# Optimization experiments

Hardware: AMD Instinct MI355X
Metric: run time of the kernel (lower is better)

## Reference

```python
import jax, jax.numpy as jnp
import numpy as np

B, MD, N = 8, 256, 4096          # batch, model_dim, n_points
H, F, S = 8, 16, 32              # heads, in_feature_dim, tensor_size (3D lattice S^3)
EPS = 1e-5


def _bn(x, g, b):
    # training-mode BatchNorm1d over (batch, points), x: [B, C, N]
    m = x.mean(axis=(0, 2), keepdims=True)
    v = x.var(axis=(0, 2), keepdims=True)
    return (x - m) * jax.lax.rsqrt(v + EPS) * g[None, :, None] + b[None, :, None]


def setup_inputs() -> dict:
    key = jax.random.key(0)
    ks = jax.random.split(key, 10)
    return {
        "x": jax.random.normal(ks[0], (B, MD, N), jnp.float32),
        "pcd": jax.random.uniform(ks[1], (B, 3, N), jnp.float32, -1.0, 1.0),
        "W_kv": jax.random.normal(ks[2], (H * (F + 3), MD), jnp.float32) / np.float32(np.sqrt(MD)),
        "key_gamma": 0.1 * jax.random.normal(ks[3], (H * 3,), jnp.float32),
        "key_beta": jnp.zeros((H * 3,), jnp.float32),
        "val_gamma": jnp.ones((H * F,), jnp.float32) + 0.1 * jax.random.normal(ks[4], (H * F,), jnp.float32),
        "val_beta": jnp.zeros((H * F,), jnp.float32),
        "R": jnp.tile(jnp.eye(3, dtype=jnp.float32), (H, 1, 1)) + 0.05 * jax.random.normal(ks[5], (H, 3, 3), jnp.float32),
        "t": 0.05 * jax.random.normal(ks[6], (H, 3), jnp.float32),
        "conv_w": jax.random.normal(ks[7], (H * F, F, 3, 3, 3), jnp.float32) / np.float32(np.sqrt(F * 27)),
        "conv_b": jnp.zeros((H * F,), jnp.float32),
        "after_gamma": jnp.ones((H * F,), jnp.float32),
        "after_beta": jnp.zeros((H * F,), jnp.float32),
    }


# precomputed 8 trilinear corner offsets
_OFFS = np.array([[dx, dy, dz] for dx in (0, 1) for dy in (0, 1) for dz in (0, 1)])
_OFF_FLAT = jnp.asarray((_OFFS[:, 0] * S + _OFFS[:, 1]) * S + _OFFS[:, 2], jnp.int32)  # [8]
_OFF_BOOL = jnp.asarray(_OFFS.astype(bool))  # [8, 3]


def _forward(x, pcd, W_kv, key_gamma, key_beta, val_gamma, val_beta, R, t,
             conv_w, conv_b, after_gamma, after_beta):
    # keys/values prediction (1x1 conv == matmul)
    kv = jnp.einsum('om,bmn->bon', W_kv, x)                      # [B, H*(F+3), N]
    keys_res = _bn(kv[:, :H * 3], key_gamma, key_beta).reshape(B, H, 3, N)
    values = _bn(kv[:, H * 3:], val_gamma, val_beta)              # [B, H*F, N]
    # per-head learned affine transform of shifted point coords (VolTransformer)
    keys = jnp.einsum('hij,bhjn->bhin', R, pcd[:, None] + keys_res) + t[None, :, :, None]
    lattice = jnp.tanh(keys)                                      # [B, H, 3, N] in (-1, 1)
    # DifferentiablePositions: map to lattice coords, split into floor index + frac
    pos = (lattice + 1.0) * 0.5 * (S - 1)
    fl_f = jnp.clip(jnp.floor(pos), 0.0, S - 2.0)
    frac = pos - fl_f                                             # differentiable local coords
    fl = fl_f.astype(jnp.int32)
    base = (fl[:, :, 0] * S + fl[:, :, 1]) * S + fl[:, :, 2]      # [B, H, N] flattened index
    idx8 = base[:, :, None, :] + _OFF_FLAT[None, None, :, None]   # [B, H, 8, N]
    # trilinear corner weights: prod_d (frac_d if corner bit else 1-frac_d)
    w8 = jnp.prod(jnp.where(_OFF_BOOL[None, None, :, :, None],
                            frac[:, :, None], 1.0 - frac[:, :, None]), axis=3)  # [B, H, 8, N]
    # Splat: weighted scatter-add onto the lattice
    vals = values.reshape(B, H, F, N)
    contrib = (vals[:, :, :, None, :] * w8[:, :, None]).reshape(B * H, F, 8 * N)
    idx_f = idx8.reshape(B * H, 8 * N)
    z = jax.vmap(lambda c, i: jnp.zeros((F, S ** 3), c.dtype).at[:, i].add(c))(contrib, idx_f)
    z = z.reshape(B, H * F, S, S, S)
    # heads-grouped 3x3x3 conv over the lattice
    zc = jax.lax.conv_general_dilated(
        z, conv_w, window_strides=(1, 1, 1), padding='SAME',
        feature_group_count=H,
        dimension_numbers=('NCDHW', 'OIDHW', 'NCDHW')) + conv_b[None, :, None, None, None]
    # Slice: gather back at the same corners with the same trilinear weights
    g = jax.vmap(lambda zf, i: zf[:, i])(zc.reshape(B * H, F, S ** 3), idx_f)  # [B*H, F, 8N]
    sliced = (g.reshape(B, H, F, 8, N) * w8[:, :, None]).sum(axis=3).reshape(B, H * F, N)
    return jax.nn.relu(_bn(sliced, after_gamma, after_beta))


def reference(x, pcd, W_kv, key_gamma, key_beta, val_gamma, val_beta, R, t,
              conv_w, conv_b, after_gamma, after_beta):
    return _forward(x, pcd, W_kv, key_gamma, key_beta, val_gamma, val_beta, R, t,
                    conv_w, conv_b, after_gamma, after_beta)
```

## Files before the change

### kernel.cpp

```cpp
#include <hip/hip_runtime.h>
#include <cstddef>
#include <cstdint>

#define BB 8
#define MD 256
#define NP 4096
#define HH 8
#define FF 16
#define SS 32
#define S3 32768
#define CC 152
#define KC 24
#define PTS (BB*HH*NP)
#define BPT (HH*NP)
#define BN_CNT (BB*NP)
#define EPSV 1e-5f
#define ZSTRH (HH*S3*FF)

typedef __attribute__((ext_vector_type(8))) short short8v;
typedef __attribute__((ext_vector_type(4))) float f32x4;

__device__ __forceinline__ unsigned int f2bf(float f) {
    unsigned int u = __float_as_uint(f);
    unsigned int r = u + 0x7FFFu + ((u >> 16) & 1u);
    return r >> 16;
}

__global__ __launch_bounds__(256) void k_wgpack(const float* __restrict__ W,
                                                unsigned short* __restrict__ wg) {
    int gid = blockIdx.x * 256 + threadIdx.x;
    if (gid >= 5120) return;
    int lane = gid & 63;
    int mc   = (gid >> 6) & 7;
    int oct  = gid >> 9;
    int oc = oct * 16 + (lane & 15);
    int m0 = mc * 32 + (lane >> 4) * 8;
    unsigned short oh[8], ol[8];
#pragma unroll
    for (int j = 0; j < 8; ++j) {
        float wv = (oc < CC) ? W[(size_t)oc * MD + m0 + j] : 0.f;
        unsigned int hi = f2bf(wv);
        float r = wv - __uint_as_float(hi << 16);
        oh[j] = (unsigned short)hi;
        ol[j] = (unsigned short)f2bf(r);
    }
    ushort4* dh = (ushort4*)(wg + (size_t)gid * 8);
    dh[0] = make_ushort4(oh[0], oh[1], oh[2], oh[3]);
    dh[1] = make_ushort4(oh[4], oh[5], oh[6], oh[7]);
    ushort4* dl = (ushort4*)(wg + (size_t)(5120 + gid) * 8);
    dl[0] = make_ushort4(ol[0], ol[1], ol[2], ol[3]);
    dl[1] = make_ushort4(ol[4], ol[5], ol[6], ol[7]);
}

__global__ __launch_bounds__(256) void k_gemm(const float* __restrict__ x,
                                              const unsigned short* __restrict__ wg,
                                              float* __restrict__ kv) {
    __shared__ __align__(16) unsigned char xh[32768];
    __shared__ __align__(16) unsigned char xlo[32768];
    int nt = blockIdx.x;
    int b  = blockIdx.y;
    int tid = threadIdx.x;
    int n_l = tid & 63, w = tid >> 6;
    int n0 = nt * 64;

    const float* xb = x + (size_t)b * MD * NP + n0;
#pragma unroll 4
    for (int k = 0; k < 32; ++k) {
        int m = k * 8 + w * 2;
        float v0 = xb[(size_t)m * NP + n_l];
        float v1 = xb[(size_t)(m + 1) * NP + n_l];
        unsigned int h0 = f2bf(v0), h1 = f2bf(v1);
        float r0 = v0 - __uint_as_float(h0 << 16);
        float r1 = v1 - __uint_as_float(h1 << 16);
        unsigned int byte = (unsigned)(n_l * 512 + m * 2) ^ (unsigned)((n_l & 7) << 4);
        *(unsigned int*)(xh + byte)  = h0 | (h1 << 16);
        *(unsigned int*)(xlo + byte) = f2bf(r0) | (f2bf(r1) << 16);
    }
    __syncthreads();

    int lane = tid & 63;
    int nn = w * 16 + (lane & 15);
    int kg = lane >> 4;
    short8v xfh[8], xfl[8];
#pragma unroll
    for (int mc = 0; mc < 8; ++mc) {
        unsigned int byte = (unsigned)(nn * 512 + (mc * 32 + kg * 8) * 2)
                          ^ (unsigned)((nn & 7) << 4);
        xfh[mc] = *(const short8v*)(xh + byte);
        xfl[mc] = *(const short8v*)(xlo + byte);
    }

    f32x4 acc[10];
#pragma unroll
    for (int t = 0; t < 10; ++t) acc[t] = (f32x4){0.f, 0.f, 0.f, 0.f};

    const short8v* wfh = (const short8v*)wg;
    const short8v* wfl = wfh + 5120;
#pragma unroll
    for (int oct = 0; oct < 10; ++oct) {
#pragma unroll
        for (int mc = 0; mc < 8; ++mc) {
            short8v wh = wfh[(oct * 8 + mc) * 64 + lane];
            short8v wl = wfl[(oct * 8 + mc) * 64 + lane];
            acc[oct] = __builtin_amdgcn_mfma_f32_16x16x32_bf16(wh, xfh[mc], acc[oct], 0, 0, 0);
            acc[oct] = __builtin_amdgcn_mfma_f32_16x16x32_bf16(wh, xfl[mc], acc[oct], 0, 0, 0);
            acc[oct] = __builtin_amdgcn_mfma_f32_16x16x32_bf16(wl, xfh[mc], acc[oct], 0, 0, 0);
        }
    }

    int n = n0 + nn;
#pragma unroll
    for (int oct = 0; oct < 10; ++oct) {
#pragma unroll
        for (int r = 0; r < 4; ++r) {
            int oc = oct * 16 + kg * 4 + r;
            if (oc < CC)
                kv[((size_t)b * CC + oc) * NP + n] = acc[oct][r];
        }
    }
}

__global__ __launch_bounds__(256) void k_stats_kv(const float* __restrict__ kv,
                                                  const float* __restrict__ kg,
                                                  const float* __restrict__ kb,
                                                  const float* __restrict__ vg,
                                                  const float* __restrict__ vb,
                                                  float* __restrict__ A,
                                                  float* __restrict__ Bv) {
    int o = blockIdx.x, tid = threadIdx.x;
    float s = 0.f, ss = 0.f;
    for (int b = 0; b < BB; ++b) {
        const float* p = kv + ((size_t)b * CC + o) * NP;
        for (int n = tid; n < NP; n += 256) { float v = p[n]; s += v; ss = fmaf(v, v, ss); }
    }
#pragma unroll
    for (int off = 32; off > 0; off >>= 1) { s += __shfl_down(s, off); ss += __shfl_down(ss, off); }
    __shared__ float sh[8];
    int lane = tid & 63, w = tid >> 6;
    if (lane == 0) { sh[w] = s; sh[4 + w] = ss; }
    __syncthreads();
    if (tid == 0) {
        float S_ = sh[0] + sh[1] + sh[2] + sh[3];
        float SSv = sh[4] + sh[5] + sh[6] + sh[7];
        float mean = S_ * (1.f / BN_CNT);
        float var  = SSv * (1.f / BN_CNT) - mean * mean;
        float rstd = rsqrtf(var + EPSV);
        float g  = (o < KC) ? kg[o] : vg[o - KC];
        float be = (o < KC) ? kb[o] : vb[o - KC];
        A[o]  = rstd * g;
        Bv[o] = be - mean * rstd * g;
    }
}

__global__ __launch_bounds__(256) void k_prep(const float* __restrict__ kv,
                                              const float* __restrict__ pcd,
                                              const float* __restrict__ A,
                                              const float* __restrict__ Bv,
                                              const float* __restrict__ R,
                                              const float* __restrict__ t,
                                              int* __restrict__ base,
                                              float* __restrict__ frac,
                                              float* __restrict__ vals) {
    int gid = blockIdx.x * 256 + threadIdx.x;
    int b = gid >> 15, h = (gid >> 12) & 7, n = gid & 4095;

    float p[3];
#pragma unroll
    for (int i = 0; i < 3; ++i) {
        int c = h * 3 + i;
        float v = kv[((size_t)b * CC + c) * NP + n];
        p[i] = pcd[((size_t)b * 3 + i) * NP + n] + fmaf(A[c], v, Bv[c]);
    }
    int fl[3]; float fr[3];
#pragma unroll
    for (int i = 0; i < 3; ++i) {
        float key = R[h * 9 + i * 3 + 0] * p[0] + R[h * 9 + i * 3 + 1] * p[1] +
                    R[h * 9 + i * 3 + 2] * p[2] + t[h * 3 + i];
        float lat = tanhf(key);
        float pos = (lat + 1.f) * 0.5f * (SS - 1);
        float flf = fminf(fmaxf(floorf(pos), 0.f), (float)(SS - 2));
        fr[i] = pos - flf;
        fl[i] = (int)flf;
    }
    base[gid] = (fl[0] * SS + fl[1]) * SS + fl[2];
    frac[gid]           = fr[0];
    frac[PTS + gid]     = fr[1];
    frac[2 * PTS + gid] = fr[2];

    float4* vo = (float4*)(vals + (size_t)gid * 16);
#pragma unroll
    for (int q = 0; q < 4; ++q) {
        float4 v;
        float* vv = (float*)&v;
#pragma unroll
        for (int j = 0; j < 4; ++j) {
            int c = KC + h * FF + q * 4 + j;
            vv[j] = fmaf(A[c], kv[((size_t)b * CC + c) * NP + n], Bv[c]);
        }
        vo[q] = v;
    }
}

__global__ __launch_bounds__(256) void k_bin(const int* __restrict__ base,
                                             const float* __restrict__ frac,
                                             int4* __restrict__ sorted,
                                             int* __restrict__ bin_start) {
    __shared__ int hist[1024];
    __shared__ int curs[1024];
    int bh = blockIdx.x;
    int tid = threadIdx.x;
    for (int k = tid; k < 1024; k += 256) hist[k] = 0;
    __syncthreads();
    int gb = bh * NP;
    for (int p = tid; p < NP; p += 256)
        atomicAdd(&hist[base[gb + p] >> 5], 1);
    __syncthreads();
    if (tid == 0) {
        int run = 0;
        for (int k = 0; k < 1024; ++k) { int c = hist[k]; hist[k] = run; run += c; }
    }
    __syncthreads();
    for (int k = tid; k < 1024; k += 256) {
        bin_start[bh * 1024 + k] = hist[k];
        curs[k] = hist[k];
    }
    __syncthreads();
    for (int p = tid; p < NP; p += 256) {
        int bs = base[gb + p];
        int slot = atomicAdd(&curs[bs >> 5], 1);
        sorted[(size_t)bh * NP + slot] =
            make_int4(p | (bs << 12),
                      __float_as_int(frac[gb + p]),
                      __float_as_int(frac[PTS + gb + p]),
                      __float_as_int(frac[2 * PTS + gb + p]));
    }
}

__global__ __launch_bounds__(256) void k_vperm(const int4* __restrict__ sorted,
                                               const float* __restrict__ vals,
                                               float* __restrict__ vals_s) {
    int gid = blockIdx.x * 256 + threadIdx.x;
    int j = gid >> 2, q = gid & 3;
    int bh = j >> 12;
    int p = sorted[j].x & 4095;
    float4 v = ((const float4*)(vals + ((size_t)bh * NP + p) * 16))[q];
    ((float4*)(vals_s + (size_t)j * 16))[q] = v;
}

__global__ __launch_bounds__(256) void k_wpack(const float* __restrict__ cw,
                                               unsigned short* __restrict__ wApack) {
    int gid = blockIdx.x * 256 + threadIdx.x;
    if (gid >= 8 * 14 * 64) return;
    int lane = gid & 63;
    int m = (gid >> 6) % 14;
    int h = gid / (14 * 64);
    int fo = lane & 15, g = lane >> 4;
    int tap = 2 * m + (g >> 1);
    int ci0 = (g & 1) * 8;
    unsigned short o[8];
#pragma unroll
    for (int j = 0; j < 8; ++j) {
        float w = (tap <= 26) ? cw[((size_t)(h * 16 + fo) * 16 + ci0 + j) * 27 + tap] : 0.f;
        o[j] = (unsigned short)f2bf(w);
    }
    ushort4* dst = (ushort4*)(wApack + (size_t)gid * 8);
    dst[0] = make_ushort4(o[0], o[1], o[2], o[3]);
    dst[1] = make_ushort4(o[4], o[5], o[6], o[7]);
}

__global__ __launch_bounds__(64) void k_splat(const int4* __restrict__ sorted,
                                              const int* __restrict__ bin_start,
                                              const float* __restrict__ vsrc,
                                              unsigned short* __restrict__ zout,
                                              int b0, int sortedVals) {
    __shared__ float zl[4][32][16];
    int x  = blockIdx.x;
    int yq = blockIdx.y;
    int hq = blockIdx.z;
    int h = hq & 7, bq = hq >> 3;
    int bh = (b0 + bq) * 8 + h;
    int lane = threadIdx.x;
    int ch = lane & 15, cor = lane >> 4;
    int dyb = cor >> 1, dzb = cor & 1;
    int row_lo = yq * 4;
    int ylo = row_lo - 1; if (ylo < 0) ylo = 0;
    int yhi = row_lo + 4;

    float4* zl4 = (float4*)zl;
    float4 zero4 = make_float4(0.f, 0.f, 0.f, 0.f);
    for (int i = lane; i < 512; i += 64) zl4[i] = zero4;
    __syncthreads();

    const int4* srt = sorted + (size_t)bh * NP;
    const float* vb = vsrc + (size_t)bh * NP * 16;
    const int* bsrt = bin_start + bh * 1024;
    int yzoff = dyb * 32 + dzb - row_lo * 32;

#pragma unroll
    for (int pass = 0; pass < 2; ++pass) {
        int s = x - 1 + pass;
        if (s < 0 || s > 30) continue;
        int j0 = bsrt[s * 32 + ylo];
        int j1 = bsrt[s * 32 + yhi];
        bool dxh = (pass == 0);
        for (int j = j0; j < j1; j += 8) {
            int4 rec[8];
            float v[8];
#pragma unroll
            for (int u = 0; u < 8; ++u) {
                int jc = j + u; jc = (jc < NP - 1) ? jc : (NP - 1);
                rec[u] = srt[jc];
            }
#pragma unroll
            for (int u = 0; u < 8; ++u) {
                int jc = j + u; jc = (jc < NP - 1) ? jc : (NP - 1);
                int vidx = sortedVals ? jc : (rec[u].x & 4095);
                v[u] = vb[(size_t)vidx * 16 + ch];
            }
#pragma unroll
            for (int u = 0; u < 8; ++u) {
                int bs = rec[u].x >> 12;
                int r = ((bs >> 5) & 31) + dyb;
                if (j + u < j1 && (unsigned)(r - row_lo) < 4u) {
                    float fx = __int_as_float(rec[u].y);
                    float fy = __int_as_float(rec[u].z);
                    float fz = __int_as_float(rec[u].w);
                    float w = (dxh ? fx : 1.f - fx) * (dyb ? fy : 1.f - fy) *
                              (dzb ? fz : 1.f - fz);
                    int addr = (bs & 1023) + yzoff;
                    (&zl[0][0][0])[addr * 16 + ch] += w * v[u];
                }
            }
        }
    }
    __syncthreads();

    for (int i = lane; i < 256; i += 64) {
        int cl = i >> 1, half = i & 1;
        float4 a = zl4[cl * 4 + half * 2];
        float4 c = zl4[cl * 4 + half * 2 + 1];
        uint4 o;
        o.x = f2bf(a.x) | (f2bf(a.y) << 16);
        o.y = f2bf(a.z) | (f2bf(a.w) << 16);
        o.z = f2bf(c.x) | (f2bf(c.y) << 16);
        o.w = f2bf(c.z) | (f2bf(c.w) << 16);
        int gcell = x * 1024 + row_lo * 32 + cl;
        *(uint4*)&zout[((size_t)(bq * HH + h) * S3 + gcell) * 16 + half * 8] = o;
    }
}

__global__ __launch_bounds__(256) void k_conv(const unsigned short* __restrict__ z,
                                              const unsigned short* __restrict__ wApack,
                                              const float* __restrict__ cb,
                                              unsigned short* __restrict__ zc) {
    __shared__ __align__(16) unsigned short zl[4][10][34][16];
    int bx = blockIdx.x;
    int yq = blockIdx.y;
    int gz = blockIdx.z;
    int h  = gz & 7;
    int bq = gz >> 3;
    int tid = threadIdx.x;
    int lane = tid & 63, wid = tid >> 6;
    int x2 = bx * 2;

    const unsigned short* zb = z + (size_t)bq * ZSTRH;
    unsigned short* zcb = zc + (size_t)bq * ZSTRH;

    short8v af[14];
    const short8v* wa = (const short8v*)(wApack + (size_t)h * 14 * 64 * 8);
#pragma unroll
    for (int m = 0; m < 14; ++m) af[m] = wa[m * 64 + lane];

    for (int i = tid; i < 4 * 10 * 34; i += 256) {
        int dxi = i / 340, rem = i % 340;
        int yy = rem / 34, zi = rem % 34;
        int gx = x2 + dxi - 1, gy = yq * 8 + yy - 1, gzz = zi - 1;
        uint4* d4 = (uint4*)(&zl[0][0][0][0] + (size_t)i * 16);
        if (gx >= 0 && gx < SS && gy >= 0 && gy < SS && gzz >= 0 && gzz < SS) {
            const uint4* src = (const uint4*)&zb[((size_t)h * S3 +
                                 (gx * 1024 + gy * 32 + gzz)) * 16];
            d4[0] = src[0];
            d4[1] = src[1];
        } else {
            uint4 zz4 = make_uint4(0, 0, 0, 0);
            d4[0] = zz4; d4[1] = zz4;
        }
    }
    __syncthreads();

    bool lo = (lane & 32) == 0;
    int ci0 = (lane & 16) ? 8 : 0;
    int l15 = lane & 15;
    int fo0 = (lane >> 4) * 4;
    float4 bias = *(const float4*)&cb[h * 16 + fo0];
    const unsigned short* zlf = &zl[0][0][0][0];

#pragma unroll 1
    for (int i = 0; i < 8; ++i) {
        int gi = wid * 8 + i;
        int xl = gi >> 4, yl = (gi >> 1) & 7, zz0 = (gi & 1) * 16;
        int invbase = xl * 340 + yl * 34 + zz0 + l15;

        f32x4 acc = {0.f, 0.f, 0.f, 0.f};
#pragma unroll
        for (int m = 0; m < 14; ++m) {
            const int t0 = 2 * m;
            const int t1 = (2 * m + 1 > 26) ? 26 : (2 * m + 1);
            const int off0 = (t0 / 9) * 340 + ((t0 % 9) / 3) * 34 + (t0 % 3);
            const int off1 = (t1 / 9) * 340 + ((t1 % 9) / 3) * 34 + (t1 % 3);
            int offc = lo ? off0 : off1;
            const short8v* bp = (const short8v*)(zlf + (size_t)(invbase + offc) * 16 + ci0);
            acc = __builtin_amdgcn_mfma_f32_16x16x32_bf16(af[m], *bp, acc, 0, 0, 0);
        }
        int cell = (x2 + xl) * 1024 + (yq * 8 + yl) * 32 + zz0 + l15;
        uint2 o;
        o.x = f2bf(acc[0] + bias.x) | (f2bf(acc[1] + bias.y) << 16);
        o.y = f2bf(acc[2] + bias.z) | (f2bf(acc[3] + bias.w) << 16);
        *(uint2*)&zcb[((size_t)h * S3 + cell) * 16 + fo0] = o;
    }
}

__global__ __launch_bounds__(256) void k_slice(const int* __restrict__ base,
                                               const float* __restrict__ frac,
                                               const unsigned short* __restrict__ zc,
                                               float* __restrict__ out, int b0) {
    int lid = blockIdx.x * 256 + threadIdx.x;
    int foq = blockIdx.y;
    int bq = blockIdx.z;
    int b = b0 + bq;
    int h = lid >> 12, n = lid & 4095;
    int gid = b * BPT + lid;
    int bs = base[gid];
    float fx = frac[gid], fy = frac[PTS + gid], fz = frac[2 * PTS + gid];
    float wx[2] = {1.f - fx, fx}, wy[2] = {1.f - fy, fy}, wz[2] = {1.f - fz, fz};
    const unsigned short* zb = zc + (size_t)bq * ZSTRH + (size_t)h * S3 * FF + foq * 4;

    float a0 = 0.f, a1 = 0.f, a2 = 0.f, a3 = 0.f;
#pragma unroll
    for (int dx = 0; dx < 2; ++dx)
#pragma unroll
    for (int dy = 0; dy < 2; ++dy)
#pragma unroll
    for (int dz = 0; dz < 2; ++dz) {
        int cell = bs + dx * (SS * SS) + dy * SS + dz;
        float w = wx[dx] * wy[dy] * wz[dz];
        uint2 u = *(const uint2*)&zb[(size_t)cell * FF];
        a0 = fmaf(__uint_as_float(u.x << 16), w, a0);
        a1 = fmaf(__uint_as_float(u.x & 0xffff0000u), w, a1);
        a2 = fmaf(__uint_as_float(u.y << 16), w, a2);
        a3 = fmaf(__uint_as_float(u.y & 0xffff0000u), w, a3);
    }
    size_t ob = ((size_t)b * (HH * FF) + h * FF + foq * 4) * NP + n;
    out[ob]          = a0;
    out[ob + NP]     = a1;
    out[ob + 2 * NP] = a2;
    out[ob + 3 * NP] = a3;
}

__global__ __launch_bounds__(256) void k_stats2(const float* __restrict__ out,
                                                const float* __restrict__ ag,
                                                const float* __restrict__ ab,
                                                float* __restrict__ A2,
                                                float* __restrict__ B2) {
    int c = blockIdx.x, tid = threadIdx.x;
    float s = 0.f, ss = 0.f;
    for (int b = 0; b < BB; ++b) {
        const float* p = out + ((size_t)b * (HH * FF) + c) * NP;
        for (int n = tid; n < NP; n += 256) { float v = p[n]; s += v; ss = fmaf(v, v, ss); }
    }
#pragma unroll
    for (int off = 32; off > 0; off >>= 1) { s += __shfl_down(s, off); ss += __shfl_down(ss, off); }
    __shared__ float sh[8];
    int lane = tid & 63, w = tid >> 6;
    if (lane == 0) { sh[w] = s; sh[4 + w] = ss; }
    __syncthreads();
    if (tid == 0) {
        float S_ = sh[0] + sh[1] + sh[2] + sh[3];
        float SSv = sh[4] + sh[5] + sh[6] + sh[7];
        float mean = S_ * (1.f / BN_CNT);
        float var  = SSv * (1.f / BN_CNT) - mean * mean;
        float rstd = rsqrtf(var + EPSV);
        A2[c] = rstd * ag[c];
        B2[c] = ab[c] - mean * rstd * ag[c];
    }
}

__global__ __launch_bounds__(256) void k_bnrelu(float* __restrict__ out,
                                                const float* __restrict__ A2,
                                                const float* __restrict__ B2) {
    int gid = blockIdx.x * 256 + threadIdx.x;
    int c = (gid >> 12) & 127;
    float v = out[gid];
    out[gid] = fmaxf(fmaf(A2[c], v, B2[c]), 0.f);
}

extern "C" void kernel_launch(void* const* d_in, const int* in_sizes, int n_in,
                              void* d_out, int out_size, void* d_ws, size_t ws_size,
                              hipStream_t stream) {
    (void)in_sizes; (void)n_in; (void)out_size;
    const float* x   = (const float*)d_in[0];
    const float* pcd = (const float*)d_in[1];
    const float* W   = (const float*)d_in[2];
    const float* kg  = (const float*)d_in[3];
    const float* kb  = (const float*)d_in[4];
    const float* vg  = (const float*)d_in[5];
    const float* vb  = (const float*)d_in[6];
    const float* R   = (const float*)d_in[7];
    const float* t   = (const float*)d_in[8];
    const float* cw  = (const float*)d_in[9];
    const float* cb  = (const float*)d_in[10];
    const float* ag  = (const float*)d_in[11];
    const float* ab  = (const float*)d_in[12];
    float* out = (float*)d_out;
    char* ws = (char*)d_ws;

    float* kv   = (float*)(ws + 0);
    int4*  sorted    = (int4*)(ws + 8388608ULL);
    int*   bin_start = (int*) (ws + 12582912ULL);
    unsigned short* wApack = (unsigned short*)(ws + 16777216ULL);
    int*   base = (int*)  (ws + 19922944ULL);
    float* frac = (float*)(ws + 20971520ULL);
    float* A    = (float*)(ws + 24117248ULL);
    float* Bv   = (float*)(ws + 24118272ULL);
    float* A2   = (float*)(ws + 24119296ULL);
    float* B2   = (float*)(ws + 24120320ULL);
    float* vals = (float*)(ws + 24121344ULL);

    int NB = 1;
    if (ws_size >= 40898560ULL + 8ULL * 16777216ULL + 16777216ULL)      NB = 8;
    else if (ws_size >= 40898560ULL + 4ULL * 16777216ULL + 16777216ULL) NB = 4;
    else if (ws_size >= 40898560ULL + 2ULL * 16777216ULL + 16777216ULL) NB = 2;

    unsigned short* z_bf;
    unsigned short* zc;
    float* vals_s = nullptr;
    int sortedVals = 1;
    if (NB == 1) {
        z_bf = (unsigned short*)kv;
        zc   = (unsigned short*)(ws + 40898560ULL);
        if (ws_size >= 57675776ULL + 16777216ULL)
            vals_s = (float*)(ws + 57675776ULL);
        else { vals_s = vals; sortedVals = 0; }
    } else {
        z_bf = (unsigned short*)(ws + 40898560ULL);
        zc   = (unsigned short*)(ws + 40898560ULL + (size_t)NB * 8388608ULL);
        vals_s = (float*)(ws + 40898560ULL + (size_t)NB * 16777216ULL);
    }
    unsigned short* wg = (unsigned short*)zc;

    k_wgpack<<<dim3(20), 256, 0, stream>>>(W, wg);
    k_gemm<<<dim3(64, BB), 256, 0, stream>>>(x, wg, kv);
    k_stats_kv<<<dim3(CC), 256, 0, stream>>>(kv, kg, kb, vg, vb, A, Bv);
    k_prep<<<dim3(PTS / 256), 256, 0, stream>>>(kv, pcd, A, Bv, R, t, base, frac, vals);
    k_bin<<<dim3(BB * HH), 256, 0, stream>>>(base, frac, sorted, bin_start);
    if (sortedVals)
        k_vperm<<<dim3(PTS * 4 / 256), 256, 0, stream>>>(sorted, vals, vals_s);
    k_wpack<<<dim3(28), 256, 0, stream>>>(cw, wApack);

    for (int b0 = 0; b0 < BB; b0 += NB) {
        k_splat<<<dim3(SS, 8, HH * NB), 64, 0, stream>>>(sorted, bin_start, vals_s,
                                                         z_bf, b0, sortedVals);
        k_conv<<<dim3(16, 4, HH * NB), 256, 0, stream>>>(z_bf, wApack, cb, zc);
        k_slice<<<dim3(BPT / 256, 4, NB), 256, 0, stream>>>(base, frac, zc, out, b0);
    }

    k_stats2<<<dim3(HH * FF), 256, 0, stream>>>(out, ag, ab, A2, B2);
    k_bnrelu<<<dim3((BB * HH * FF * NP) / 256), 256, 0, stream>>>(out, A2, B2);
}
```

Before: 315.4 us.

## Store sorted splat values in bf16 and slice all 16 features per thread

The value permutation kernel now writes the sorted per-point values as bf16 instead of fp32. This halves the buffer that the splat kernel gathers from, and the unsorted fallback path is removed so the sorted buffer is always used. The slice kernel now has each thread read all 16 channels of a corner cell with two 16-byte loads, replacing four grid slices that each recomputed the index and weights for 4 channels. The changes trade some value precision (bf16 rounding before splatting) and higher register use in the slice kernel for less memory traffic and fewer redundant loads.

```diff
diff --git a/kernel.cpp b/kernel.cpp
--- a/kernel.cpp
+++ b/kernel.cpp
@@ -238,13 +238,19 @@
 
 __global__ __launch_bounds__(256) void k_vperm(const int4* __restrict__ sorted,
                                                const float* __restrict__ vals,
-                                               float* __restrict__ vals_s) {
+                                               unsigned short* __restrict__ vals_s) {
     int gid = blockIdx.x * 256 + threadIdx.x;
-    int j = gid >> 2, q = gid & 3;
+    int j = gid >> 1, half = gid & 1;
     int bh = j >> 12;
     int p = sorted[j].x & 4095;
-    float4 v = ((const float4*)(vals + ((size_t)bh * NP + p) * 16))[q];
-    ((float4*)(vals_s + (size_t)j * 16))[q] = v;
+    const float4* src = (const float4*)(vals + ((size_t)bh * NP + p) * 16) + half * 2;
+    float4 a = src[0], c = src[1];
+    uint4 o;
+    o.x = f2bf(a.x) | (f2bf(a.y) << 16);
+    o.y = f2bf(a.z) | (f2bf(a.w) << 16);
+    o.z = f2bf(c.x) | (f2bf(c.y) << 16);
+    o.w = f2bf(c.z) | (f2bf(c.w) << 16);
+    *(uint4*)(vals_s + (size_t)j * 16 + half * 8) = o;
 }
 
 __global__ __launch_bounds__(256) void k_wpack(const float* __restrict__ cw,
@@ -270,9 +276,9 @@
 
 __global__ __launch_bounds__(64) void k_splat(const int4* __restrict__ sorted,
                                               const int* __restrict__ bin_start,
-                                              const float* __restrict__ vsrc,
+                                              const unsigned short* __restrict__ vsrc,
                                               unsigned short* __restrict__ zout,
-                                              int b0, int sortedVals) {
+                                              int b0) {
     __shared__ float zl[4][32][16];
     int x  = blockIdx.x;
     int yq = blockIdx.y;
@@ -292,7 +298,7 @@
     __syncthreads();
 
     const int4* srt = sorted + (size_t)bh * NP;
-    const float* vb = vsrc + (size_t)bh * NP * 16;
+    const unsigned short* vb = vsrc + (size_t)bh * NP * 16;
     const int* bsrt = bin_start + bh * 1024;
     int yzoff = dyb * 32 + dzb - row_lo * 32;
 
@@ -314,8 +320,7 @@
 #pragma unroll
             for (int u = 0; u < 8; ++u) {
                 int jc = j + u; jc = (jc < NP - 1) ? jc : (NP - 1);
-                int vidx = sortedVals ? jc : (rec[u].x & 4095);
-                v[u] = vb[(size_t)vidx * 16 + ch];
+                v[u] = __uint_as_float((unsigned)vb[(size_t)jc * 16 + ch] << 16);
             }
 #pragma unroll
             for (int u = 0; u < 8; ++u) {
@@ -425,17 +430,18 @@
                                                const unsigned short* __restrict__ zc,
                                                float* __restrict__ out, int b0) {
     int lid = blockIdx.x * 256 + threadIdx.x;
-    int foq = blockIdx.y;
-    int bq = blockIdx.z;
+    int bq = blockIdx.y;
     int b = b0 + bq;
     int h = lid >> 12, n = lid & 4095;
     int gid = b * BPT + lid;
     int bs = base[gid];
     float fx = frac[gid], fy = frac[PTS + gid], fz = frac[2 * PTS + gid];
     float wx[2] = {1.f - fx, fx}, wy[2] = {1.f - fy, fy}, wz[2] = {1.f - fz, fz};
-    const unsigned short* zb = zc + (size_t)bq * ZSTRH + (size_t)h * S3 * FF + foq * 4;
-
-    float a0 = 0.f, a1 = 0.f, a2 = 0.f, a3 = 0.f;
+    const unsigned short* zb = zc + (size_t)bq * ZSTRH + (size_t)h * S3 * FF;
+
+    float acc[16];
+#pragma unroll
+    for (int f = 0; f < 16; ++f) acc[f] = 0.f;
 #pragma unroll
     for (int dx = 0; dx < 2; ++dx)
 #pragma unroll
@@ -444,17 +450,30 @@
     for (int dz = 0; dz < 2; ++dz) {
         int cell = bs + dx * (SS * SS) + dy * SS + dz;
         float w = wx[dx] * wy[dy] * wz[dz];
-        uint2 u = *(const uint2*)&zb[(size_t)cell * FF];
-        a0 = fmaf(__uint_as_float(u.x << 16), w, a0);
-        a1 = fmaf(__uint_as_float(u.x & 0xffff0000u), w, a1);
-        a2 = fmaf(__uint_as_float(u.y << 16), w, a2);
-        a3 = fmaf(__uint_as_float(u.y & 0xffff0000u), w, a3);
-    }
-    size_t ob = ((size_t)b * (HH * FF) + h * FF + foq * 4) * NP + n;
-    out[ob]          = a0;
-    out[ob + NP]     = a1;
-    out[ob + 2 * NP] = a2;
-    out[ob + 3 * NP] = a3;
+        const uint4* src = (const uint4*)&zb[(size_t)cell * 16];
+        uint4 u0 = src[0];
+        uint4 u1 = src[1];
+        acc[0]  = fmaf(__uint_as_float(u0.x << 16), w, acc[0]);
+        acc[1]  = fmaf(__uint_as_float(u0.x & 0xffff0000u), w, acc[1]);
+        acc[2]  = fmaf(__uint_as_float(u0.y << 16), w, acc[2]);
+        acc[3]  = fmaf(__uint_as_float(u0.y & 0xffff0000u), w, acc[3]);
+        acc[4]  = fmaf(__uint_as_float(u0.z << 16), w, acc[4]);
+        acc[5]  = fmaf(__uint_as_float(u0.z & 0xffff0000u), w, acc[5]);
+        acc[6]  = fmaf(__uint_as_float(u0.w << 16), w, acc[6]);
+        acc[7]  = fmaf(__uint_as_float(u0.w & 0xffff0000u), w, acc[7]);
+        acc[8]  = fmaf(__uint_as_float(u1.x << 16), w, acc[8]);
+        acc[9]  = fmaf(__uint_as_float(u1.x & 0xffff0000u), w, acc[9]);
+        acc[10] = fmaf(__uint_as_float(u1.y << 16), w, acc[10]);
+        acc[11] = fmaf(__uint_as_float(u1.y & 0xffff0000u), w, acc[11]);
+        acc[12] = fmaf(__uint_as_float(u1.z << 16), w, acc[12]);
+        acc[13] = fmaf(__uint_as_float(u1.z & 0xffff0000u), w, acc[13]);
+        acc[14] = fmaf(__uint_as_float(u1.w << 16), w, acc[14]);
+        acc[15] = fmaf(__uint_as_float(u1.w & 0xffff0000u), w, acc[15]);
+    }
+    size_t ob = ((size_t)b * (HH * FF) + h * FF) * NP + n;
+#pragma unroll
+    for (int f = 0; f < 16; ++f)
+        out[ob + (size_t)f * NP] = acc[f];
 }
 
 __global__ __launch_bounds__(256) void k_stats2(const float* __restrict__ out,
@@ -527,24 +546,21 @@
     float* vals = (float*)(ws + 24121344ULL);
 
     int NB = 1;
-    if (ws_size >= 40898560ULL + 8ULL * 16777216ULL + 16777216ULL)      NB = 8;
-    else if (ws_size >= 40898560ULL + 4ULL * 16777216ULL + 16777216ULL) NB = 4;
-    else if (ws_size >= 40898560ULL + 2ULL * 16777216ULL + 16777216ULL) NB = 2;
+    if (ws_size >= 40898560ULL + 8ULL * 16777216ULL + 8388608ULL)      NB = 8;
+    else if (ws_size >= 40898560ULL + 4ULL * 16777216ULL + 8388608ULL) NB = 4;
+    else if (ws_size >= 40898560ULL + 2ULL * 16777216ULL + 8388608ULL) NB = 2;
 
     unsigned short* z_bf;
     unsigned short* zc;
-    float* vals_s = nullptr;
-    int sortedVals = 1;
+    unsigned short* vals_s;
     if (NB == 1) {
         z_bf = (unsigned short*)kv;
         zc   = (unsigned short*)(ws + 40898560ULL);
-        if (ws_size >= 57675776ULL + 16777216ULL)
-            vals_s = (float*)(ws + 57675776ULL);
-        else { vals_s = vals; sortedVals = 0; }
+        vals_s = (unsigned short*)(ws + 49287168ULL);
     } else {
         z_bf = (unsigned short*)(ws + 40898560ULL);
         zc   = (unsigned short*)(ws + 40898560ULL + (size_t)NB * 8388608ULL);
-        vals_s = (float*)(ws + 40898560ULL + (size_t)NB * 16777216ULL);
+        vals_s = (unsigned short*)(ws + 40898560ULL + (size_t)NB * 16777216ULL);
     }
     unsigned short* wg = (unsigned short*)zc;
 
@@ -553,15 +569,14 @@
     k_stats_kv<<<dim3(CC), 256, 0, stream>>>(kv, kg, kb, vg, vb, A, Bv);
     k_prep<<<dim3(PTS / 256), 256, 0, stream>>>(kv, pcd, A, Bv, R, t, base, frac, vals);
     k_bin<<<dim3(BB * HH), 256, 0, stream>>>(base, frac, sorted, bin_start);
-    if (sortedVals)
-        k_vperm<<<dim3(PTS * 4 / 256), 256, 0, stream>>>(sorted, vals, vals_s);
+    k_vperm<<<dim3(PTS * 2 / 256), 256, 0, stream>>>(sorted, vals, vals_s);
     k_wpack<<<dim3(28), 256, 0, stream>>>(cw, wApack);
 
     for (int b0 = 0; b0 < BB; b0 += NB) {
         k_splat<<<dim3(SS, 8, HH * NB), 64, 0, stream>>>(sorted, bin_start, vals_s,
-                                                         z_bf, b0, sortedVals);
+                                                         z_bf, b0);
         k_conv<<<dim3(16, 4, HH * NB), 256, 0, stream>>>(z_bf, wApack, cb, zc);
-        k_slice<<<dim3(BPT / 256, 4, NB), 256, 0, stream>>>(base, frac, zc, out, b0);
+        k_slice<<<dim3(BPT / 256, NB), 256, 0, stream>>>(base, frac, zc, out, b0);
     }
 
     k_stats2<<<dim3(HH * FF), 256, 0, stream>>>(out, ag, ab, A2, B2);
```

Result: faster. 303.6 us (-3.7%).
